# Kernel optimization log

Hardware: AMD Instinct MI355X
Metric: run time of the kernel (lower is better)

## Reference

```python
import jax, jax.numpy as jnp
import numpy as np

FP, DP, K, S, B, T, H, ZD = 96, 28, 3, 4, 64, 8, 512, 2
CP = FP - DP + 1          # 69, valid cross-correlation output size
NP = CP * CP              # 4761 = num_pixels


def setup_inputs() -> dict:
    key = jax.random.key(0)
    ks = jax.random.split(key, 12)
    def rn(k, shape, s=0.02):
        return jax.random.normal(k, shape, jnp.float32) * s
    return {
        "frames": jax.random.uniform(ks[0], (S, B, T, FP, FP), jnp.float32),
        "conv_kernel": jax.random.uniform(ks[1], (S, B, K, DP, DP), jnp.float32),
        "eps": jax.random.normal(ks[2], (S, B, K, ZD), jnp.float32),
        "W1": rn(ks[3], (NP, H)), "b1": jnp.zeros((H,), jnp.float32),
        "Wm1": rn(ks[4], (H, H // 2)), "bm1": jnp.zeros((H // 2,), jnp.float32),
        "Wm2": rn(ks[5], (H // 2, ZD)), "bm2": jnp.zeros((ZD,), jnp.float32),
        "Ws1": rn(ks[6], (H, H // 2)), "bs1": jnp.zeros((H // 2,), jnp.float32),
        "Ws2": rn(ks[7], (H // 2, ZD)), "bs2": jnp.zeros((ZD,), jnp.float32),
        "timestep": 0,
    }


def _axis_weights(p, n):
    """Bilinear 1-D gather indices/weights with zero padding outside [0, n)."""
    p0 = jnp.floor(p)
    f = p - p0
    i0 = p0.astype(jnp.int32)
    i1 = i0 + 1
    w0 = jnp.where((i0 >= 0) & (i0 < n), 1.0 - f, 0.0)
    w1 = jnp.where((i1 >= 0) & (i1 < n), f, 0.0)
    return jnp.clip(i0, 0, n - 1), jnp.clip(i1, 0, n - 1), w0, w1


def _place_digit(digit, zw):
    """AT.digit_to_frame: place DPxDP digit into FPxFP frame at z_where (torch
    affine_grid/grid_sample, align_corners=False, zero padding). theta scale =
    FP/DP, translation = -z_where*FP/DP, i.e. in_coord = (FP/DP)*(out - zw)."""
    scale = FP / DP
    out_c = (2.0 * jnp.arange(FP, dtype=jnp.float32) + 1.0) / FP - 1.0  # (FP,)
    px = ((scale * (out_c - zw[0]) + 1.0) * DP - 1.0) * 0.5  # x source pix
    py = ((scale * (out_c - zw[1]) + 1.0) * DP - 1.0) * 0.5  # y source pix
    y0, y1, wy0, wy1 = _axis_weights(py, DP)
    x0, x1, wx0, wx1 = _axis_weights(px, DP)
    # separable bilinear: interp rows then cols
    tmp = wy0[:, None] * digit[y0, :] + wy1[:, None] * digit[y1, :]  # (FP,DP)
    return wx0[None, :] * tmp[:, x0] + wx1[None, :] * tmp[:, x1]     # (FP,FP)

_place_batch = jax.vmap(_place_digit)


def reference(frames, conv_kernel, eps, W1, b1, Wm1, bm1, Wm2, bm2,
              Ws1, bs1, Ws2, bs2, timestep):
    SB = S * B
    frame_left = frames[:, :, timestep]  # (S,B,FP,FP)
    means, stds, zs = [], [], []
    for k in range(K):
        # per-sample dynamic-kernel cross-correlation via grouped conv
        lhs = frame_left.reshape(1, SB, FP, FP)
        rhs = conv_kernel[:, :, k].reshape(SB, 1, DP, DP)
        conved = jax.lax.conv_general_dilated(
            lhs, rhs, (1, 1), 'VALID', feature_group_count=SB)  # (1,SB,CP,CP)
        scores = jax.nn.softmax(conved.reshape(S, B, NP), axis=-1)
        h = jax.nn.relu(scores @ W1 + b1)                       # (S,B,H)
        mean_k = jnp.tanh(jax.nn.relu(h @ Wm1 + bm1) @ Wm2 + bm2)
        std_k = jnp.exp(jax.nn.relu(h @ Ws1 + bs1) @ Ws2 + bs2)
        z_k = mean_k + std_k * eps[:, :, k]                     # rsample
        recon = _place_batch(conv_kernel[:, :, k].reshape(SB, DP, DP),
                             z_k.reshape(SB, ZD)).reshape(S, B, FP, FP)
        frame_left = frame_left - recon
        means.append(mean_k); stds.append(std_k); zs.append(z_k)
    q_mean = jnp.stack(means, 2)    # (S,B,K,2)
    q_std = jnp.stack(stds, 2)
    z_where = jnp.stack(zs, 2)
    return jnp.stack([q_mean, q_std, z_where], 0)  # (3,S,B,K,2)
```

## Files before the change

kernel.cpp:

```cpp
#include <hip/hip_runtime.h>
#include <hip/hip_bf16.h>
#include <math.h>

#define FPD 96
#define DPD 28
#define CPD 69
#define NPD 4761
#define KKC 3
#define SBN 256
#define TT 8
#define HD 512
#define ZDD 2
#define KP2 5120
#define HALFK 2560
#define SPLITK 16
#define FRSH 104
#define CVS 76

typedef __attribute__((ext_vector_type(8))) short bf16x8;
typedef __attribute__((ext_vector_type(4))) float f32x4;
typedef _Float16 half_t;
typedef __attribute__((ext_vector_type(2))) _Float16 half2_t;

__device__ __forceinline__ float bf2f_lo(unsigned int u) {
    union { unsigned int i; float f; } v; v.i = u << 16; return v.f;
}
__device__ __forceinline__ float bf2f_hi(unsigned int u) {
    union { unsigned int i; float f; } v; v.i = u & 0xffff0000u; return v.f;
}
__device__ __forceinline__ half2_t u2h(unsigned int u) {
    union { unsigned int i; half2_t h; } v; v.i = u; return v.h;
}

struct ConvLds {
    half_t fr[62 * FRSH];
    half_t kr[28 * 32];
    float  dg[2][784];
    float  cv[4][35 * CVS];
    float  red[32];
};

struct MlpLds {
    float hsh[HD];
    float h2[2][256];
    float res_sh[2][2];
};

__device__ __forceinline__ float recon_val(
    const float* __restrict__ dg, float zx, float zy, int r, int c)
{
    const float scale = 96.f / 28.f;
    float oci = (2.f * r + 1.f) / 96.f - 1.f;
    float ocj = (2.f * c + 1.f) / 96.f - 1.f;
    float py = ((scale * (oci - zy) + 1.f) * 28.f - 1.f) * 0.5f;
    float px = ((scale * (ocj - zx) + 1.f) * 28.f - 1.f) * 0.5f;
    float py0f = floorf(py), px0f = floorf(px);
    float fy = py - py0f, fx = px - px0f;
    int y0 = (int)py0f, x0 = (int)px0f;
    int y1 = y0 + 1, x1 = x0 + 1;
    float wy0 = (y0 >= 0 && y0 < DPD) ? 1.f - fy : 0.f;
    float wy1 = (y1 >= 0 && y1 < DPD) ? fy : 0.f;
    float wx0 = (x0 >= 0 && x0 < DPD) ? 1.f - fx : 0.f;
    float wx1 = (x1 >= 0 && x1 < DPD) ? fx : 0.f;
    int y0c = min(max(y0, 0), DPD - 1), y1c = min(max(y1, 0), DPD - 1);
    int x0c = min(max(x0, 0), DPD - 1), x1c = min(max(x1, 0), DPD - 1);
    float tmp0 = wy0 * dg[y0c * DPD + x0c] + wy1 * dg[y1c * DPD + x0c];
    float tmp1 = wy0 * dg[y0c * DPD + x1c] + wy1 * dg[y1c * DPD + x1c];
    return wx0 * tmp0 + wx1 * tmp1;
}

__device__ __forceinline__ void stage_kernel_rows(
    ConvLds& L, const float* __restrict__ ck, int ib, int k, int t)
{
    if (t < 28 * 32) {
        int dy = t >> 5, dx = t & 31;
        float v = (dx < 28) ? ck[((size_t)ib * KKC + k) * 784 + dy * 28 + dx] : 0.f;
        L.kr[t] = (half_t)v;
    }
}

template<int NREC>
__device__ __forceinline__ void conv_rest(
    ConvLds& L, int ib, int half, int t,
    const float* __restrict__ pf,
    float z0x, float z0y, float z1x, float z1y,
    ushort* __restrict__ e_buf, float* __restrict__ stats_w)
{
    half_t* fr  = L.fr;
    float*  red = L.red;
    const int roy0  = half ? 35 : 0;
    const int nrows = half ? 61 : 62;
    const int oycnt = half ? 34 : 35;
    const int lim   = nrows * 96;

    #pragma unroll
    for (int i = 0; i < 6; ++i) {
        int p = t + i * 1024;
        if (p < lim) {
            int lr = p / 96, c = p - lr * 96;
            int r = roy0 + lr;
            float val = pf[i];
            if (NREC >= 1) val -= recon_val(L.dg[0], z0x, z0y, r, c);
            if (NREC >= 2) val -= recon_val(L.dg[1], z1x, z1y, r, c);
            fr[lr * FRSH + c] = (half_t)val;
        }
    }
    if (t < 62 * 8) fr[(t >> 3) * FRSH + 96 + (t & 7)] = (half_t)0.f;
    __syncthreads();

    const int NT = 12 * oycnt;
    if (t < NT) {
        const int q    = t / (3 * oycnt);
        const int rem  = t - q * (3 * oycnt);
        const int tile = rem / oycnt;
        const int oyl  = rem - tile * oycnt;
        const int ox0  = tile * 24;
        const int dy0  = q * 7;

        float acc[24];
        #pragma unroll
        for (int j = 0; j < 24; ++j) acc[j] = 0.f;

        #pragma unroll 1
        for (int dd = 0; dd < 7; ++dd) {
            const int dy = dy0 + dd;
            const unsigned int* frow = (const unsigned int*)&fr[(oyl + dy) * FRSH + ox0];
            const unsigned int* krow = (const unsigned int*)&L.kr[dy * 32];
            unsigned int W[28], K[16], V[25];
            #pragma unroll
            for (int u = 0; u < 7; ++u) {
                uint4 v = *(const uint4*)(frow + 4 * u);
                W[4*u] = v.x; W[4*u+1] = v.y; W[4*u+2] = v.z; W[4*u+3] = v.w;
            }
            #pragma unroll
            for (int u = 0; u < 4; ++u) {
                uint4 v = *(const uint4*)(krow + 4 * u);
                K[4*u] = v.x; K[4*u+1] = v.y; K[4*u+2] = v.z; K[4*u+3] = v.w;
            }
            #pragma unroll
            for (int i = 0; i < 25; ++i)
                V[i] = (W[i] >> 16) | (W[i + 1] << 16);
            #pragma unroll
            for (int m = 0; m < 12; ++m) {
                float ae = acc[2*m], ao = acc[2*m+1];
                #pragma unroll
                for (int i = 0; i < 14; ++i) {
                    ae = __builtin_amdgcn_fdot2(u2h(W[m + i]), u2h(K[i]), ae, false);
                    ao = __builtin_amdgcn_fdot2(u2h(V[m + i]), u2h(K[i]), ao, false);
                }
                acc[2*m] = ae; acc[2*m+1] = ao;
            }
        }
        float* cvq = &L.cv[q][oyl * CVS + ox0];
        #pragma unroll
        for (int u = 0; u < 6; ++u) {
            float4 v = make_float4(acc[4*u], acc[4*u+1], acc[4*u+2], acc[4*u+3]);
            *(float4*)(cvq + 4 * u) = v;
        }
    }
    __syncthreads();

    const int nele = oycnt * CVS;
    float m = -INFINITY;
    for (int p = t; p < nele; p += 1024) {
        int ox = p - (p / CVS) * CVS;
        if (ox < CPD) {
            float v = L.cv[0][p] + L.cv[1][p] + L.cv[2][p] + L.cv[3][p];
            L.cv[0][p] = v;
            m = fmaxf(m, v);
        }
    }
    #pragma unroll
    for (int off = 32; off > 0; off >>= 1) m = fmaxf(m, __shfl_down(m, off, 64));
    int lane = t & 63, wid = t >> 6;
    if (lane == 0) red[wid] = m;
    __syncthreads();
    m = red[0];
    #pragma unroll
    for (int i = 1; i < 16; ++i) m = fmaxf(m, red[i]);

    const int kbase = half ? HALFK : 0;
    float s = 0.f;
    ushort* eo = e_buf + (size_t)ib * KP2;
    for (int p = t; p < nele; p += 1024) {
        int oyl = p / CVS;
        int ox = p - oyl * CVS;
        if (ox < CPD) {
            float ev = __expf(L.cv[0][p] - m);
            __hip_bfloat16 h = __float2bfloat16(ev);
            eo[kbase + oyl * 69 + ox] = *reinterpret_cast<ushort*>(&h);
            s += ev;
        }
    }
    #pragma unroll
    for (int off = 32; off > 0; off >>= 1) s += __shfl_down(s, off, 64);
    if (lane == 0) red[16 + wid] = s;
    __syncthreads();
    if (t == 0) {
        float tot = 0.f;
        #pragma unroll
        for (int i = 0; i < 16; ++i) tot += red[16 + i];
        stats_w[ib * 4 + half * 2]     = m;
        stats_w[ib * 4 + half * 2 + 1] = tot;
    }
    const int padbase = half ? (HALFK + 34 * 69) : (35 * 69);
    const int padcnt  = half ? (KP2 - (HALFK + 34 * 69)) : (HALFK - 35 * 69);
    if (t < padcnt) eo[padbase + t] = 0;
}

__device__ __forceinline__ void mlp_phase(
    MlpLds& L, int km, int ib, int t,
    float csum, float invd, float b1v,
    const ushort* __restrict__ WhidT,
    const float* __restrict__ bm1, const float* __restrict__ bs1,
    const float* __restrict__ Wm2, const float* __restrict__ bm2,
    const float* __restrict__ Ws2, const float* __restrict__ bs2,
    const float* __restrict__ eps, float* __restrict__ out,
    float* z_keep)
{
    if (t < HD)
        L.hsh[t] = fmaxf(fmaf(csum, invd, b1v), 0.f);
    __syncthreads();

    if (t < 512) {
        int head = t >> 8, col = t & 255;
        const uint4* Wr = (const uint4*)(WhidT + (size_t)(head * 256 + col) * 512);
        float bias = head ? bs1[col] : bm1[col];
        float a = 0.f;
        #pragma unroll 8
        for (int u = 0; u < 64; ++u) {
            uint4 wv = Wr[u];
            const float* hp = &L.hsh[u * 8];
            a = fmaf(hp[0], bf2f_lo(wv.x), a);
            a = fmaf(hp[1], bf2f_hi(wv.x), a);
            a = fmaf(hp[2], bf2f_lo(wv.y), a);
            a = fmaf(hp[3], bf2f_hi(wv.y), a);
            a = fmaf(hp[4], bf2f_lo(wv.z), a);
            a = fmaf(hp[5], bf2f_hi(wv.z), a);
            a = fmaf(hp[6], bf2f_lo(wv.w), a);
            a = fmaf(hp[7], bf2f_hi(wv.w), a);
        }
        L.h2[head][col] = fmaxf(a + bias, 0.f);
    }
    __syncthreads();

    {
        int w = t >> 6, l = t & 63;
        if (w < 4) {
            int zd = (w >> 1) & 1, head = w & 1;
            const float* W2 = head ? Ws2 : Wm2;
            float a = 0.f;
            #pragma unroll
            for (int u = 0; u < 4; ++u) {
                int i = l + u * 64;
                a = fmaf(L.h2[head][i], W2[i * 2 + zd], a);
            }
            #pragma unroll
            for (int off = 32; off > 0; off >>= 1) a += __shfl_down(a, off, 64);
            if (l == 0) {
                float r = head ? __expf(a + bs2[zd]) : tanhf(a + bm2[zd]);
                L.res_sh[zd][head] = r;
            }
        }
    }
    __syncthreads();
    if (t < 2) {
        int zd = t;
        float mean = L.res_sh[zd][0];
        float stdv = L.res_sh[zd][1];
        float ev = eps[(size_t)ib * 6 + km * 2 + zd];
        float z = fmaf(stdv, ev, mean);
        int oidx = ib * 6 + km * 2 + zd;
        out[oidx]        = mean;
        out[1536 + oidx] = stdv;
        out[3072 + oidx] = z;
        z_keep[zd] = z;
    }
}

__device__ __forceinline__ void mlp_inputs(
    const float* __restrict__ Cpart, const float* __restrict__ stats_r,
    const float* __restrict__ b1, int ib, int t,
    float& csum, float& invd, float& b1v)
{
    float c0 = 0.f, c1 = 0.f;
    b1v = 0.f;
    if (t < HD) {
        #pragma unroll
        for (int z = 0; z < 8; ++z)
            c0 += Cpart[((size_t)ib * SPLITK + z) * HD + t];
        #pragma unroll
        for (int z = 8; z < 16; ++z)
            c1 += Cpart[((size_t)ib * SPLITK + z) * HD + t];
        b1v = b1[t];
    }
    float M0 = stats_r[ib * 4 + 0], S0 = stats_r[ib * 4 + 1];
    float M1 = stats_r[ib * 4 + 2], S1 = stats_r[ib * 4 + 3];
    float M  = fmaxf(M0, M1);
    float f0 = __expf(M0 - M), f1 = __expf(M1 - M);
    invd = 1.f / fmaf(S0, f0, S1 * f1);
    csum = fmaf(c0, f0, c1 * f1);
}

__global__ __launch_bounds__(1024, 8) void conv0_wprep_kernel(
    const float* __restrict__ frames, const int* __restrict__ tsp,
    const float* __restrict__ ck,
    ushort* __restrict__ e_buf, float* __restrict__ stats0,
    const float* __restrict__ W1, const float* __restrict__ Wm1,
    const float* __restrict__ Ws1,
    ushort* __restrict__ W1T, ushort* __restrict__ WhidT)
{
    __shared__ union __align__(16) {
        ConvLds conv;
        ushort wp[4][64][65];
    } sh;
    const int t    = threadIdx.x;
    const int ibh  = blockIdx.x;
    const int ib   = ibh >> 1;
    const int half = ibh & 1;

    const int roy0 = half ? 35 : 0;
    const int lim  = (half ? 61 : 62) * 96;
    const float* src = frames + ((size_t)ib * TT + *tsp) * 9216 + roy0 * 96;
    float pf[6];
    #pragma unroll
    for (int i = 0; i < 6; ++i) {
        int p = t + i * 1024;
        pf[i] = (p < lim) ? src[p] : 0.f;
    }
    stage_kernel_rows(sh.conv, ck, ib, 0, t);
    __syncthreads();

    conv_rest<0>(sh.conv, ib, half, t, pf, 0.f, 0.f, 0.f, 0.f, e_buf, stats0);
    __syncthreads();

    {
        const int g  = t >> 8;
        const int tt = t & 255;
        const int ln = tt & 63;
        const int lr = tt >> 6;
        const int b  = ibh * 4 + g;
        ushort (*tile)[65] = sh.wp[g];

        if (b < 640) {
            const int k0 = (b % 80) * 64;
            const int n0 = (b / 80) * 64;
            #pragma unroll
            for (int i = 0; i < 16; ++i) {
                int kk = k0 + lr + i * 4;
                int np = (kk < HALFK) ? kk : kk - 145;
                bool ok = (kk < 2415) || (kk >= HALFK && kk < 4906);
                float v = ok ? W1[(size_t)np * HD + n0 + ln] : 0.f;
                __hip_bfloat16 h = __float2bfloat16(v);
                tile[lr + i * 4][ln] = *reinterpret_cast<ushort*>(&h);
            }
        } else if (b < 704) {
            const int bb = b - 640;
            const int i0 = (bb & 7) * 64;
            const int r0 = (bb >> 3) * 64;
            #pragma unroll
            for (int rep = 0; rep < 16; ++rep) {
                int i = i0 + lr + rep * 4;
                int r = r0 + ln;
                const float* srcp = (r >= 256) ? Ws1 : Wm1;
                float v = srcp[(size_t)i * 256 + (r & 255)];
                __hip_bfloat16 h = __float2bfloat16(v);
                tile[lr + rep * 4][ln] = *reinterpret_cast<ushort*>(&h);
            }
        }
        __syncthreads();
        if (b < 640) {
            const int k0 = (b % 80) * 64;
            const int n0 = (b / 80) * 64;
            #pragma unroll
            for (int i = 0; i < 16; ++i) {
                int nn = lr + i * 4;
                int kk = k0 + ln;
                W1T[(size_t)(n0 + nn) * KP2 + kk] = tile[ln][nn];
            }
        } else if (b < 704) {
            const int bb = b - 640;
            const int i0 = (bb & 7) * 64;
            const int r0 = (bb >> 3) * 64;
            #pragma unroll
            for (int rep = 0; rep < 16; ++rep) {
                int r = r0 + lr + rep * 4;
                WhidT[(size_t)r * 512 + i0 + ln] = tile[ln][lr + rep * 4];
            }
        }
    }
}

#define GLOADSET(A,B0,B1,B2,B3,OFF)                        \
    A  = *(const bf16x8*)(pA + (OFF));                     \
    B0 = *(const bf16x8*)(pB + (OFF));                     \
    B1 = *(const bf16x8*)(pB + 16 * KP2 + (OFF));          \
    B2 = *(const bf16x8*)(pB + 32 * KP2 + (OFF));          \
    B3 = *(const bf16x8*)(pB + 48 * KP2 + (OFF));

__global__ __launch_bounds__(64) void gemm1_mfma(
    const ushort* __restrict__ E, const ushort* __restrict__ W1T,
    float* __restrict__ Cpart)
{
    const int t  = threadIdx.x;
    const int bx = blockIdx.x;
    const int n0 = blockIdx.y * 64;
    const int z  = blockIdx.z;

    const int lm = t & 15;
    const int kb = (t & 63) >> 4;

    f32x4 zero = {0.f, 0.f, 0.f, 0.f};
    f32x4 acc[4] = {zero, zero, zero, zero};

    const ushort* pA = E   + (size_t)(bx * 16 + lm) * KP2 + kb * 8;
    const ushort* pB = W1T + (size_t)(n0 + lm) * KP2 + kb * 8;
    const int kk0 = z * 320;

    bf16x8 a0, b00, b01, b02, b03;
    bf16x8 a1, b10, b11, b12, b13;
    GLOADSET(a0, b00, b01, b02, b03, kk0)
    GLOADSET(a1, b10, b11, b12, b13, kk0 + 32)

    #pragma unroll 1
    for (int s = 0; s < 10; s += 2) {
        bf16x8 ca = a0, c0 = b00, c1 = b01, c2 = b02, c3 = b03;
        if (s + 2 < 10) { int kn = kk0 + (s + 2) * 32;
            GLOADSET(a0, b00, b01, b02, b03, kn) }
        acc[0] = __builtin_amdgcn_mfma_f32_16x16x32_bf16(ca, c0, acc[0], 0, 0, 0);
        acc[1] = __builtin_amdgcn_mfma_f32_16x16x32_bf16(ca, c1, acc[1], 0, 0, 0);
        acc[2] = __builtin_amdgcn_mfma_f32_16x16x32_bf16(ca, c2, acc[2], 0, 0, 0);
        acc[3] = __builtin_amdgcn_mfma_f32_16x16x32_bf16(ca, c3, acc[3], 0, 0, 0);

        bf16x8 da = a1, d0 = b10, d1 = b11, d2 = b12, d3 = b13;
        if (s + 3 < 10) { int kn = kk0 + (s + 3) * 32;
            GLOADSET(a1, b10, b11, b12, b13, kn) }
        acc[0] = __builtin_amdgcn_mfma_f32_16x16x32_bf16(da, d0, acc[0], 0, 0, 0);
        acc[1] = __builtin_amdgcn_mfma_f32_16x16x32_bf16(da, d1, acc[1], 0, 0, 0);
        acc[2] = __builtin_amdgcn_mfma_f32_16x16x32_bf16(da, d2, acc[2], 0, 0, 0);
        acc[3] = __builtin_amdgcn_mfma_f32_16x16x32_bf16(da, d3, acc[3], 0, 0, 0);
    }

    const int mrow = bx * 16 + kb * 4;
    #pragma unroll
    for (int j = 0; j < 4; ++j) {
        int n = n0 + j * 16 + lm;
        #pragma unroll
        for (int rg = 0; rg < 4; ++rg)
            Cpart[((size_t)(mrow + rg) * SPLITK + z) * HD + n] = acc[j][rg];
    }
}

template<int KM>
__global__ __launch_bounds__(1024, 8) void mlp_conv_kernel(
    const float* __restrict__ Cpart, const float* __restrict__ stats_r,
    float* __restrict__ stats_w,
    const float* __restrict__ b1, const ushort* __restrict__ WhidT,
    const float* __restrict__ bm1, const float* __restrict__ bs1,
    const float* __restrict__ Wm2, const float* __restrict__ bm2,
    const float* __restrict__ Ws2, const float* __restrict__ bs2,
    const float* __restrict__ eps, float* __restrict__ out,
    const float* __restrict__ frames, const int* __restrict__ tsp,
    const float* __restrict__ ck, ushort* __restrict__ e_buf)
{
    __shared__ union __align__(16) {
        ConvLds conv;
        MlpLds  mlp;
    } sh;
    __shared__ float z_keep[2];
    const int t    = threadIdx.x;
    const int ibh  = blockIdx.x;
    const int ib   = ibh >> 1;
    const int half = ibh & 1;

    const int roy0 = half ? 35 : 0;
    const int lim  = (half ? 61 : 62) * 96;
    const float* src = frames + ((size_t)ib * TT + *tsp) * 9216 + roy0 * 96;
    float pf[6];
    #pragma unroll
    for (int i = 0; i < 6; ++i) {
        int p = t + i * 1024;
        pf[i] = (p < lim) ? src[p] : 0.f;
    }
    stage_kernel_rows(sh.conv, ck, ib, KM + 1, t);
    if (t < 784) {
        sh.conv.dg[0][t] = ck[((size_t)ib * KKC + 0) * 784 + t];
        if (KM == 1)
            sh.conv.dg[1][t] = ck[((size_t)ib * KKC + 1) * 784 + t];
    }
    float z0x = 0.f, z0y = 0.f;
    if (KM == 1) {
        z0x = out[3072 + ib * 6 + 0];
        z0y = out[3072 + ib * 6 + 1];
    }
    float csum, invd, b1v;
    mlp_inputs(Cpart, stats_r, b1, ib, t, csum, invd, b1v);

    mlp_phase(sh.mlp, KM, ib, t, csum, invd, b1v, WhidT,
              bm1, bs1, Wm2, bm2, Ws2, bs2, eps, out, z_keep);
    __syncthreads();

    float zkx = z_keep[0], zky = z_keep[1];
    if (KM == 0) {
        conv_rest<1>(sh.conv, ib, half, t, pf, zkx, zky, 0.f, 0.f,
                     e_buf, stats_w);
    } else {
        conv_rest<2>(sh.conv, ib, half, t, pf, z0x, z0y, zkx, zky,
                     e_buf, stats_w);
    }
}

__global__ __launch_bounds__(512) void mlp_final_kernel(
    const float* __restrict__ Cpart, const float* __restrict__ stats_r,
    const float* __restrict__ b1, const ushort* __restrict__ WhidT,
    const float* __restrict__ bm1, const float* __restrict__ bs1,
    const float* __restrict__ Wm2, const float* __restrict__ bm2,
    const float* __restrict__ Ws2, const float* __restrict__ bs2,
    const float* __restrict__ eps, float* __restrict__ out)
{
    __shared__ MlpLds L;
    __shared__ float z_keep[2];
    const int t  = threadIdx.x;
    const int ib = blockIdx.x;
    float csum, invd, b1v;
    mlp_inputs(Cpart, stats_r, b1, ib, t, csum, invd, b1v);
    mlp_phase(L, 2, ib, t, csum, invd, b1v, WhidT,
              bm1, bs1, Wm2, bm2, Ws2, bs2, eps, out, z_keep);
}

extern "C" void kernel_launch(void* const* d_in, const int* in_sizes, int n_in,
                              void* d_out, int out_size, void* d_ws, size_t ws_size,
                              hipStream_t stream)
{
    const float* frames = (const float*)d_in[0];
    const float* ck     = (const float*)d_in[1];
    const float* eps    = (const float*)d_in[2];
    const float* W1     = (const float*)d_in[3];
    const float* b1     = (const float*)d_in[4];
    const float* Wm1    = (const float*)d_in[5];
    const float* bm1    = (const float*)d_in[6];
    const float* Wm2    = (const float*)d_in[7];
    const float* bm2    = (const float*)d_in[8];
    const float* Ws1    = (const float*)d_in[9];
    const float* bs1    = (const float*)d_in[10];
    const float* Ws2    = (const float*)d_in[11];
    const float* bs2    = (const float*)d_in[12];
    const int*   tsp    = (const int*)d_in[13];
    float* out = (float*)d_out;

    float* Cpart   = (float*)d_ws;
    float* statsA  = Cpart + 2097152;
    float* statsB  = statsA + 1024;
    ushort* e_buf  = (ushort*)(statsB + 1024);
    ushort* W1T    = e_buf + (size_t)SBN * KP2;
    ushort* WhidT  = W1T + (size_t)HD * KP2;

    conv0_wprep_kernel<<<512, 1024, 0, stream>>>(
        frames, tsp, ck, e_buf, statsA, W1, Wm1, Ws1, W1T, WhidT);
    gemm1_mfma<<<dim3(16, 8, SPLITK), 64, 0, stream>>>(e_buf, W1T, Cpart);
    mlp_conv_kernel<0><<<512, 1024, 0, stream>>>(
        Cpart, statsA, statsB, b1, WhidT, bm1, bs1, Wm2, bm2, Ws2, bs2,
        eps, out, frames, tsp, ck, e_buf);
    gemm1_mfma<<<dim3(16, 8, SPLITK), 64, 0, stream>>>(e_buf, W1T, Cpart);
    mlp_conv_kernel<1><<<512, 1024, 0, stream>>>(
        Cpart, statsB, statsA, b1, WhidT, bm1, bs1, Wm2, bm2, Ws2, bs2,
        eps, out, frames, tsp, ck, e_buf);
    gemm1_mfma<<<dim3(16, 8, SPLITK), 64, 0, stream>>>(e_buf, W1T, Cpart);
    mlp_final_kernel<<<256, 512, 0, stream>>>(
        Cpart, statsA, b1, WhidT, bm1, bs1, Wm2, bm2, Ws2, bs2, eps, out);
}
```

Baseline: 335.7 us.

## Halve conv/MLP block size to 512 threads and drop frame prefetch registers

The fused conv and MLP kernels now launch with 512 threads per block instead of 1024, and every strided loop and reduction is adjusted to match. The frame pixels are no longer prefetched into registers at kernel start. They are read from global memory directly inside the residual-frame fill, which cuts register pressure. The weight-prep portion of the first kernel now handles two tiles per block instead of four. The risk is less latency hiding: the frame loads are no longer overlapped with the MLP phase, and each thread now runs more loop iterations.

```diff
diff --git a/kernel.cpp b/kernel.cpp
--- a/kernel.cpp
+++ b/kernel.cpp
@@ -72,17 +72,17 @@
 __device__ __forceinline__ void stage_kernel_rows(
     ConvLds& L, const float* __restrict__ ck, int ib, int k, int t)
 {
-    if (t < 28 * 32) {
-        int dy = t >> 5, dx = t & 31;
+    for (int p = t; p < 28 * 32; p += 512) {
+        int dy = p >> 5, dx = p & 31;
         float v = (dx < 28) ? ck[((size_t)ib * KKC + k) * 784 + dy * 28 + dx] : 0.f;
-        L.kr[t] = (half_t)v;
+        L.kr[p] = (half_t)v;
     }
 }
 
 template<int NREC>
 __device__ __forceinline__ void conv_rest(
     ConvLds& L, int ib, int half, int t,
-    const float* __restrict__ pf,
+    const float* __restrict__ src,
     float z0x, float z0y, float z1x, float z1y,
     ushort* __restrict__ e_buf, float* __restrict__ stats_w)
 {
@@ -94,12 +94,12 @@
     const int lim   = nrows * 96;
 
     #pragma unroll
-    for (int i = 0; i < 6; ++i) {
-        int p = t + i * 1024;
+    for (int i = 0; i < 12; ++i) {
+        int p = t + i * 512;
         if (p < lim) {
             int lr = p / 96, c = p - lr * 96;
             int r = roy0 + lr;
-            float val = pf[i];
+            float val = src[p];
             if (NREC >= 1) val -= recon_val(L.dg[0], z0x, z0y, r, c);
             if (NREC >= 2) val -= recon_val(L.dg[1], z1x, z1y, r, c);
             fr[lr * FRSH + c] = (half_t)val;
@@ -162,7 +162,7 @@
 
     const int nele = oycnt * CVS;
     float m = -INFINITY;
-    for (int p = t; p < nele; p += 1024) {
+    for (int p = t; p < nele; p += 512) {
         int ox = p - (p / CVS) * CVS;
         if (ox < CPD) {
             float v = L.cv[0][p] + L.cv[1][p] + L.cv[2][p] + L.cv[3][p];
@@ -177,12 +177,12 @@
     __syncthreads();
     m = red[0];
     #pragma unroll
-    for (int i = 1; i < 16; ++i) m = fmaxf(m, red[i]);
+    for (int i = 1; i < 8; ++i) m = fmaxf(m, red[i]);
 
     const int kbase = half ? HALFK : 0;
     float s = 0.f;
     ushort* eo = e_buf + (size_t)ib * KP2;
-    for (int p = t; p < nele; p += 1024) {
+    for (int p = t; p < nele; p += 512) {
         int oyl = p / CVS;
         int ox = p - oyl * CVS;
         if (ox < CPD) {
@@ -199,7 +199,7 @@
     if (t == 0) {
         float tot = 0.f;
         #pragma unroll
-        for (int i = 0; i < 16; ++i) tot += red[16 + i];
+        for (int i = 0; i < 8; ++i) tot += red[16 + i];
         stats_w[ib * 4 + half * 2]     = m;
         stats_w[ib * 4 + half * 2 + 1] = tot;
     }
@@ -218,11 +218,10 @@
     const float* __restrict__ eps, float* __restrict__ out,
     float* z_keep)
 {
-    if (t < HD)
-        L.hsh[t] = fmaxf(fmaf(csum, invd, b1v), 0.f);
-    __syncthreads();
-
-    if (t < 512) {
+    L.hsh[t] = fmaxf(fmaf(csum, invd, b1v), 0.f);
+    __syncthreads();
+
+    {
         int head = t >> 8, col = t & 255;
         const uint4* Wr = (const uint4*)(WhidT + (size_t)(head * 256 + col) * 512);
         float bias = head ? bs1[col] : bm1[col];
@@ -284,16 +283,13 @@
     float& csum, float& invd, float& b1v)
 {
     float c0 = 0.f, c1 = 0.f;
-    b1v = 0.f;
-    if (t < HD) {
-        #pragma unroll
-        for (int z = 0; z < 8; ++z)
-            c0 += Cpart[((size_t)ib * SPLITK + z) * HD + t];
-        #pragma unroll
-        for (int z = 8; z < 16; ++z)
-            c1 += Cpart[((size_t)ib * SPLITK + z) * HD + t];
-        b1v = b1[t];
-    }
+    #pragma unroll
+    for (int z = 0; z < 8; ++z)
+        c0 += Cpart[((size_t)ib * SPLITK + z) * HD + t];
+    #pragma unroll
+    for (int z = 8; z < 16; ++z)
+        c1 += Cpart[((size_t)ib * SPLITK + z) * HD + t];
+    b1v = b1[t];
     float M0 = stats_r[ib * 4 + 0], S0 = stats_r[ib * 4 + 1];
     float M1 = stats_r[ib * 4 + 2], S1 = stats_r[ib * 4 + 3];
     float M  = fmaxf(M0, M1);
@@ -302,7 +298,7 @@
     csum = fmaf(c0, f0, c1 * f1);
 }
 
-__global__ __launch_bounds__(1024, 8) void conv0_wprep_kernel(
+__global__ __launch_bounds__(512, 4) void conv0_wprep_kernel(
     const float* __restrict__ frames, const int* __restrict__ tsp,
     const float* __restrict__ ck,
     ushort* __restrict__ e_buf, float* __restrict__ stats0,
@@ -312,7 +308,7 @@
 {
     __shared__ union __align__(16) {
         ConvLds conv;
-        ushort wp[4][64][65];
+        ushort wp[2][64][65];
     } sh;
     const int t    = threadIdx.x;
     const int ibh  = blockIdx.x;
@@ -320,18 +316,11 @@
     const int half = ibh & 1;
 
     const int roy0 = half ? 35 : 0;
-    const int lim  = (half ? 61 : 62) * 96;
     const float* src = frames + ((size_t)ib * TT + *tsp) * 9216 + roy0 * 96;
-    float pf[6];
-    #pragma unroll
-    for (int i = 0; i < 6; ++i) {
-        int p = t + i * 1024;
-        pf[i] = (p < lim) ? src[p] : 0.f;
-    }
     stage_kernel_rows(sh.conv, ck, ib, 0, t);
     __syncthreads();
 
-    conv_rest<0>(sh.conv, ib, half, t, pf, 0.f, 0.f, 0.f, 0.f, e_buf, stats0);
+    conv_rest<0>(sh.conv, ib, half, t, src, 0.f, 0.f, 0.f, 0.f, e_buf, stats0);
     __syncthreads();
 
     {
@@ -339,7 +328,7 @@
         const int tt = t & 255;
         const int ln = tt & 63;
         const int lr = tt >> 6;
-        const int b  = ibh * 4 + g;
+        const int b  = ibh * 2 + g;
         ushort (*tile)[65] = sh.wp[g];
 
         if (b < 640) {
@@ -452,7 +441,7 @@
 }
 
 template<int KM>
-__global__ __launch_bounds__(1024, 8) void mlp_conv_kernel(
+__global__ __launch_bounds__(512, 4) void mlp_conv_kernel(
     const float* __restrict__ Cpart, const float* __restrict__ stats_r,
     float* __restrict__ stats_w,
     const float* __restrict__ b1, const ushort* __restrict__ WhidT,
@@ -473,20 +462,11 @@
     const int ib   = ibh >> 1;
     const int half = ibh & 1;
 
-    const int roy0 = half ? 35 : 0;
-    const int lim  = (half ? 61 : 62) * 96;
-    const float* src = frames + ((size_t)ib * TT + *tsp) * 9216 + roy0 * 96;
-    float pf[6];
-    #pragma unroll
-    for (int i = 0; i < 6; ++i) {
-        int p = t + i * 1024;
-        pf[i] = (p < lim) ? src[p] : 0.f;
-    }
     stage_kernel_rows(sh.conv, ck, ib, KM + 1, t);
-    if (t < 784) {
-        sh.conv.dg[0][t] = ck[((size_t)ib * KKC + 0) * 784 + t];
+    for (int p = t; p < 784; p += 512) {
+        sh.conv.dg[0][p] = ck[((size_t)ib * KKC + 0) * 784 + p];
         if (KM == 1)
-            sh.conv.dg[1][t] = ck[((size_t)ib * KKC + 1) * 784 + t];
+            sh.conv.dg[1][p] = ck[((size_t)ib * KKC + 1) * 784 + p];
     }
     float z0x = 0.f, z0y = 0.f;
     if (KM == 1) {
@@ -500,12 +480,14 @@
               bm1, bs1, Wm2, bm2, Ws2, bs2, eps, out, z_keep);
     __syncthreads();
 
+    const int roy0 = half ? 35 : 0;
+    const float* src = frames + ((size_t)ib * TT + *tsp) * 9216 + roy0 * 96;
     float zkx = z_keep[0], zky = z_keep[1];
     if (KM == 0) {
-        conv_rest<1>(sh.conv, ib, half, t, pf, zkx, zky, 0.f, 0.f,
+        conv_rest<1>(sh.conv, ib, half, t, src, zkx, zky, 0.f, 0.f,
                      e_buf, stats_w);
     } else {
-        conv_rest<2>(sh.conv, ib, half, t, pf, z0x, z0y, zkx, zky,
+        conv_rest<2>(sh.conv, ib, half, t, src, z0x, z0y, zkx, zky,
                      e_buf, stats_w);
     }
 }
@@ -555,14 +537,14 @@
     ushort* W1T    = e_buf + (size_t)SBN * KP2;
     ushort* WhidT  = W1T + (size_t)HD * KP2;
 
-    conv0_wprep_kernel<<<512, 1024, 0, stream>>>(
+    conv0_wprep_kernel<<<512, 512, 0, stream>>>(
         frames, tsp, ck, e_buf, statsA, W1, Wm1, Ws1, W1T, WhidT);
     gemm1_mfma<<<dim3(16, 8, SPLITK), 64, 0, stream>>>(e_buf, W1T, Cpart);
-    mlp_conv_kernel<0><<<512, 1024, 0, stream>>>(
+    mlp_conv_kernel<0><<<512, 512, 0, stream>>>(
         Cpart, statsA, statsB, b1, WhidT, bm1, bs1, Wm2, bm2, Ws2, bs2,
         eps, out, frames, tsp, ck, e_buf);
     gemm1_mfma<<<dim3(16, 8, SPLITK), 64, 0, stream>>>(e_buf, W1T, Cpart);
-    mlp_conv_kernel<1><<<512, 1024, 0, stream>>>(
+    mlp_conv_kernel<1><<<512, 512, 0, stream>>>(
         Cpart, statsB, statsA, b1, WhidT, bm1, bs1, Wm2, bm2, Ws2, bs2,
         eps, out, frames, tsp, ck, e_buf);
     gemm1_mfma<<<dim3(16, 8, SPLITK), 64, 0, stream>>>(e_buf, W1T, Cpart);
```

New measurement: 342.8 us. 1.02x slower.
